# Kernel tuning notes

Measured on AMD Instinct MI355X. Metric: run time of the kernel, lower is better.

The kernel has to match this reference:

```python
import jax, jax.numpy as jnp
import numpy as np

B, T, H, I, O, R = 64, 1024, 1024, 8, 8, 4
NOISE_STD, ALPHA = 0.05, 0.2


def setup_inputs() -> dict:
    key = jax.random.key(0)
    ks = jax.random.split(key, 6)
    return {
        "x": jax.random.normal(ks[0], (B, T, I), jnp.float32),
        "noise": jax.random.normal(ks[1], (B, T, H), jnp.float32),
        "wi": jax.random.normal(ks[2], (I, H), jnp.float32),
        "si": jnp.ones((I,), jnp.float32),
        "m": jax.random.normal(ks[3], (H, R), jnp.float32),
        "n": jax.random.normal(ks[4], (H, R), jnp.float32),
        "b": jnp.zeros((H,), jnp.float32),
        "wo": jax.random.normal(ks[5], (H, O), jnp.float32) / H,
        "so": jnp.ones((O,), jnp.float32),
        "h0": jnp.zeros((H,), jnp.float32),
    }


def reference(x, noise, wi, si, m, n, b, wo, so, h0):
    hidden = h0.shape[0]
    batch = x.shape[0]
    wi_full = wi * si[:, None]          # (I, H): (wi.T * si).T
    wo_full = wo * so                   # (H, O)
    h_init = jnp.broadcast_to(h0, (batch, hidden))
    r_init = jnp.tanh(h_init)           # non_linearity(initial_states)
    # precompute input drive for all steps: (B,T,H) -> scan over time-major
    u = jnp.einsum('bti,ih->tbh', x, wi_full)
    noise_t = jnp.transpose(noise, (1, 0, 2))  # (T,B,H)

    def step(carry, inp):
        h, r = carry
        u_i, nz_i = inp
        rec = (r @ n) @ m.T / hidden                    # low-rank recurrence
        h = h + NOISE_STD * nz_i + ALPHA * (-h + rec + u_i)
        r = jnp.tanh(h + b)
        out = h @ wo_full                               # identity output nonlin
        return (h, r), out

    _, outs = jax.lax.scan(step, (h_init, r_init), (u, noise_t))
    return jnp.transpose(outs, (1, 0, 2))  # (B,T,O)
```

## Files before the change

### kernel.cpp

```cpp
#include <hip/hip_runtime.h>

#define BB 64
#define TT 1024
#define HH 1024
#define II 8
#define OO 8
#define RRK 4
#define NOISE_STD 0.05f
#define ALPHA 0.2f

typedef float v4f __attribute__((ext_vector_type(4)));

#define C2E 2.885390081777927f

template<int CTRL, int RM>
__device__ __forceinline__ float dpp_add(float acc, float src) {
    int s = __builtin_amdgcn_update_dpp(0, __float_as_int(src), CTRL, RM, 0xF, true);
    return acc + __int_as_float(s);
}

__device__ __forceinline__ float wave_sum(float x) {
    x = dpp_add<0xB1, 0xF>(x, x);
    x = dpp_add<0x4E, 0xF>(x, x);
    x = dpp_add<0x141, 0xF>(x, x);
    x = dpp_add<0x140, 0xF>(x, x);
    x = dpp_add<0x142, 0xA>(x, x);
    x = dpp_add<0x143, 0xC>(x, x);
    return x;
}

__device__ __forceinline__ float tanh_from_l2x(float l2x) {
    float e = __builtin_amdgcn_exp2f(l2x);
    float r = __builtin_amdgcn_rcpf(e + 1.0f);
    return fmaf(-2.0f, r, 1.0f);
}

__device__ __forceinline__ void block_sync_lds() {
    asm volatile("s_waitcnt lgkmcnt(0)\n\ts_barrier" ::: "memory");
}

__global__ __launch_bounds__(256)
void prew_kernel(const float* __restrict__ noise, const float* __restrict__ wo,
                 const float* __restrict__ so, float* __restrict__ W) {
    __shared__ __align__(16) float red[2][8][4][8];

    const int tid  = threadIdx.x;
    const int wave = tid >> 6;
    const int lane = tid & 63;
    const int e0   = tid << 2;

    float woa[4][OO];
    {
        float so8[OO];
        #pragma unroll
        for (int o = 0; o < OO; ++o) so8[o] = so[o] * NOISE_STD;
        #pragma unroll
        for (int e = 0; e < 4; ++e) {
            const float4 a4 = *(const float4*)(wo + (e0 + e) * OO);
            const float4 b4 = *(const float4*)(wo + (e0 + e) * OO + 4);
            woa[e][0] = a4.x * so8[0]; woa[e][1] = a4.y * so8[1];
            woa[e][2] = a4.z * so8[2]; woa[e][3] = a4.w * so8[3];
            woa[e][4] = b4.x * so8[4]; woa[e][5] = b4.y * so8[5];
            woa[e][6] = b4.z * so8[6]; woa[e][7] = b4.w * so8[7];
        }
    }

    const int row0 = blockIdx.x * 32;
    #pragma unroll
    for (int ph = 0; ph < 4; ++ph) {
        const int cur   = ph & 1;
        const int rbase = row0 + ph * 8;

        float4 nz[8];
        #pragma unroll
        for (int j = 0; j < 8; ++j)
            nz[j] = *(const float4*)(noise + (size_t)(rbase + j) * HH + e0);

        #pragma unroll
        for (int j = 0; j < 8; ++j) {
            float op[OO];
            #pragma unroll
            for (int o = 0; o < OO; ++o)
                op[o] = fmaf(nz[j].x, woa[0][o], fmaf(nz[j].y, woa[1][o],
                        fmaf(nz[j].z, woa[2][o], nz[j].w * woa[3][o])));
            #pragma unroll
            for (int o = 0; o < OO; ++o) op[o] = wave_sum(op[o]);
            if (lane == 63) {
                *(float4*)&red[cur][j][wave][0] = make_float4(op[0], op[1], op[2], op[3]);
                *(float4*)&red[cur][j][wave][4] = make_float4(op[4], op[5], op[6], op[7]);
            }
        }
        block_sync_lds();
        if (tid < 64) {
            const int j = tid >> 3, o = tid & 7;
            W[(rbase + j) * OO + o] = (red[cur][j][0][o] + red[cur][j][1][o]) +
                                      (red[cur][j][2][o] + red[cur][j][3][o]);
        }
    }
}

__global__ __launch_bounds__(256, 1)
void rnn_seq_kernel(const float* __restrict__ x, const float* __restrict__ noise,
                    const float* __restrict__ wi, const float* __restrict__ si,
                    const float* __restrict__ mM, const float* __restrict__ nM,
                    const float* __restrict__ bv, const float* __restrict__ wo,
                    const float* __restrict__ so, const float* __restrict__ h0,
                    const float* __restrict__ W, float* __restrict__ out) {
    __shared__ __align__(16) float lds_x[(TT + 1) * II];
    __shared__ __align__(16) float lds_W[TT * OO];
    __shared__ __align__(16) float lds_out[TT * OO];
    __shared__ __align__(16) float red[4][4][4];
    __shared__ __align__(16) float redc[4][104];
    __shared__ float ambx[104];

    const int tid  = threadIdx.x;
    const int b    = blockIdx.x;
    const int wave = tid >> 6;
    const int lane = tid & 63;
    const int e0   = tid << 2;
    const int oc   = tid & 7;

    {
        const float4* sx = (const float4*)(x + (size_t)b * (TT * II));
        const float4* sw = (const float4*)(W + (size_t)b * (TT * OO));
        float4* dx = (float4*)lds_x;
        float4* dw = (float4*)lds_W;
        #pragma unroll
        for (int k = 0; k < 8; ++k) {
            dx[k * 256 + tid] = sx[k * 256 + tid];
            dw[k * 256 + tid] = sw[k * 256 + tid];
        }
        if (tid < 2) dx[2048 + tid] = sx[2046 + tid];
    }

    float wia[II][4];
    v4f   wiac[II];
    #pragma unroll
    for (int i = 0; i < II; ++i) {
        const float s  = ALPHA * si[i];
        const float4 w = *(const float4*)(wi + i * HH + e0);
        wia[i][0] = w.x * s; wia[i][1] = w.y * s; wia[i][2] = w.z * s; wia[i][3] = w.w * s;
        wiac[i] = (v4f){wia[i][0], wia[i][1], wia[i][2], wia[i][3]};
    }
    float ma[4][RRK];
    v4f   nrv[4];
    v4f   mac[RRK];
    #pragma unroll
    for (int e = 0; e < 4; ++e) {
        const float4 m4 = *(const float4*)(mM + (e0 + e) * RRK);
        const float4 n4 = *(const float4*)(nM + (e0 + e) * RRK);
        const float cs = ALPHA / (float)HH;
        ma[e][0] = m4.x * cs; ma[e][1] = m4.y * cs; ma[e][2] = m4.z * cs; ma[e][3] = m4.w * cs;
        nrv[e] = (v4f){n4.x, n4.y, n4.z, n4.w};
    }
    #pragma unroll
    for (int q = 0; q < RRK; ++q)
        mac[q] = (v4f){ma[0][q], ma[1][q], ma[2][q], ma[3][q]};

    float woa[4][OO];
    {
        float so8[OO];
        #pragma unroll
        for (int o = 0; o < OO; ++o) so8[o] = so[o];
        #pragma unroll
        for (int e = 0; e < 4; ++e) {
            const float4 a4 = *(const float4*)(wo + (e0 + e) * OO);
            const float4 b4 = *(const float4*)(wo + (e0 + e) * OO + 4);
            woa[e][0] = a4.x * so8[0]; woa[e][1] = a4.y * so8[1];
            woa[e][2] = a4.z * so8[2]; woa[e][3] = a4.w * so8[3];
            woa[e][4] = b4.x * so8[4]; woa[e][5] = b4.y * so8[5];
            woa[e][6] = b4.z * so8[6]; woa[e][7] = b4.w * so8[7];
        }
    }
    v4f tb2e, h, r;
    {
        const v4f b4 = *(const v4f*)(bv + e0);
        tb2e = C2E * b4;
        h = *(const v4f*)(h0 + e0);
        v4f targ = C2E * h;
        r.x = tanh_from_l2x(targ.x); r.y = tanh_from_l2x(targ.y);
        r.z = tanh_from_l2x(targ.z); r.w = tanh_from_l2x(targ.w);
    }

    #pragma unroll
    for (int kg = 0; kg < 26; ++kg) {
        float p[4];
        #pragma unroll
        for (int u = 0; u < 4; ++u) {
            const int k = kg * 4 + u;
            float s;
            if (k < 32) {
                const int q = k >> 3, o = k & 7;
                s = fmaf(ma[0][q], woa[0][o], fmaf(ma[1][q], woa[1][o],
                    fmaf(ma[2][q], woa[2][o], ma[3][q] * woa[3][o])));
            } else if (k < 96) {
                const int i = (k - 32) >> 3, o = k & 7;
                s = fmaf(wia[i][0], woa[0][o], fmaf(wia[i][1], woa[1][o],
                    fmaf(wia[i][2], woa[2][o], wia[i][3] * woa[3][o])));
            } else {
                const int o = k - 96;
                s = fmaf(h.x, woa[0][o], fmaf(h.y, woa[1][o],
                    fmaf(h.z, woa[2][o], h.w * woa[3][o])));
            }
            p[u] = wave_sum(s);
        }
        if (lane == 63)
            *(float4*)&redc[wave][kg * 4] = make_float4(p[0], p[1], p[2], p[3]);
    }
    block_sync_lds();
    if (tid < 104)
        ambx[tid] = (redc[0][tid] + redc[1][tid]) + (redc[2][tid] + redc[3][tid]);
    __syncthreads();

    float Amr[RRK], Bxr[II], y;
    #pragma unroll
    for (int q = 0; q < RRK; ++q) Amr[q] = ambx[q * 8 + oc];
    #pragma unroll
    for (int i = 0; i < II; ++i) Bxr[i] = ambx[32 + i * 8 + oc];
    y = ambx[96 + oc];

    const float* nzp = noise + (size_t)b * (TT * HH) + e0;
    v4f nzb[4];
    #pragma unroll
    for (int j = 0; j < 4; ++j) nzb[j] = *(const v4f*)(nzp + j * HH);

    v4f xqc0 = *(const v4f*)&lds_x[0];
    v4f xqc1 = *(const v4f*)&lds_x[4];
    float wqc = lds_W[oc];

    for (int t0 = 0; t0 < TT; t0 += 4) {
        #pragma unroll
        for (int j = 0; j < 4; ++j) {
            const int t = t0 + j;

            const int tn = t + 1;
            const v4f xqn0 = *(const v4f*)&lds_x[tn * II];
            const v4f xqn1 = *(const v4f*)&lds_x[tn * II + 4];
            const float wqn = lds_W[(tn & (TT - 1)) * OO + oc];

            v4f vpv = r.x * nrv[0];
            vpv += r.y * nrv[1];
            vpv += r.z * nrv[2];
            vpv += r.w * nrv[3];
            float vp0 = wave_sum(vpv.x);
            float vp1 = wave_sum(vpv.y);
            float vp2 = wave_sum(vpv.z);
            float vp3 = wave_sum(vpv.w);
            if (lane == 63)
                *(float4*)&red[j][wave][0] = make_float4(vp0, vp1, vp2, vp3);

            float ybase = fmaf(xqc0.x, Bxr[0], wqc);
            ybase = fmaf(xqc0.y, Bxr[1], ybase);
            ybase = fmaf(xqc0.z, Bxr[2], ybase);
            ybase = fmaf(xqc0.w, Bxr[3], ybase);
            ybase = fmaf(xqc1.x, Bxr[4], ybase);
            ybase = fmaf(xqc1.y, Bxr[5], ybase);
            ybase = fmaf(xqc1.z, Bxr[6], ybase);
            ybase = fmaf(xqc1.w, Bxr[7], ybase);

            v4f auv = xqc0.x * wiac[0];
            auv += xqc0.y * wiac[1];
            auv += xqc0.z * wiac[2];
            auv += xqc0.w * wiac[3];
            auv += xqc1.x * wiac[4];
            auv += xqc1.y * wiac[5];
            auv += xqc1.z * wiac[6];
            auv += xqc1.w * wiac[7];

            block_sync_lds();

            const v4f s0 = *(const v4f*)&red[j][0][0];
            const v4f s1 = *(const v4f*)&red[j][1][0];
            const v4f s2 = *(const v4f*)&red[j][2][0];
            const v4f s3 = *(const v4f*)&red[j][3][0];
            const v4f vs = (s0 + s1) + (s2 + s3);

            v4f acc = auv;
            acc += vs.x * mac[0];
            acc += vs.y * mac[1];
            acc += vs.z * mac[2];
            acc += vs.w * mac[3];
            h = (1.0f - ALPHA) * h + acc;
            h += NOISE_STD * nzb[j];

            {
                float t4 = fmaf(vs.x, Amr[0], ybase);
                t4 = fmaf(vs.y, Amr[1], t4);
                t4 = fmaf(vs.z, Amr[2], t4);
                t4 = fmaf(vs.w, Amr[3], t4);
                y = fmaf(1.0f - ALPHA, y, t4);
                if (tid < OO) lds_out[t * OO + tid] = y;
            }

            nzb[j] = *(const v4f*)(nzp + ((t + 4) & (TT - 1)) * HH);

            {
                v4f targ = C2E * h + tb2e;
                r.x = tanh_from_l2x(targ.x);
                r.y = tanh_from_l2x(targ.y);
                r.z = tanh_from_l2x(targ.z);
                r.w = tanh_from_l2x(targ.w);
            }

            xqc0 = xqn0; xqc1 = xqn1; wqc = wqn;
        }
    }

    __syncthreads();
    {
        float4* dst = (float4*)(out + (size_t)b * (TT * OO));
        const float4* srcv = (const float4*)lds_out;
        #pragma unroll
        for (int k = 0; k < 8; ++k)
            dst[k * 256 + tid] = srcv[k * 256 + tid];
    }
}

extern "C" void kernel_launch(void* const* d_in, const int* in_sizes, int n_in,
                              void* d_out, int out_size, void* d_ws, size_t ws_size,
                              hipStream_t stream) {
    const float* x     = (const float*)d_in[0];
    const float* noise = (const float*)d_in[1];
    const float* wi    = (const float*)d_in[2];
    const float* si    = (const float*)d_in[3];
    const float* mM    = (const float*)d_in[4];
    const float* nM    = (const float*)d_in[5];
    const float* bv    = (const float*)d_in[6];
    const float* wo    = (const float*)d_in[7];
    const float* so    = (const float*)d_in[8];
    const float* h0    = (const float*)d_in[9];
    float* out = (float*)d_out;
    float* W   = (float*)d_ws;

    prew_kernel<<<dim3(2048), dim3(256), 0, stream>>>(noise, wo, so, W);
    rnn_seq_kernel<<<dim3(BB), dim3(256), 0, stream>>>(
        x, noise, wi, si, mM, nM, bv, wo, so, h0, W, out);
}
```

Baseline: 769.7 us.

## Double sequential kernel threads to 512, two hidden units each; prefetch noise in prew

The recurrent kernel now runs 512 threads per batch block, with each thread owning 2 hidden units instead of 4. The cross-wave reduction grows from 4 to 8 partial sums. This halves the per-thread serial work per timestep, mainly the tanh calls and the vector FMAs, and doubles the waves available to hide the per-step noise loads. The cost is an extra LDS read and add per step for the larger reduction, plus more waves taking part in each barrier. Separately, prew_kernel now loads the next phase's noise rows before it reduces the current ones, to overlap that memory traffic with compute.

```diff
diff --git a/kernel.cpp b/kernel.cpp
--- a/kernel.cpp
+++ b/kernel.cpp
@@ -10,6 +10,7 @@
 #define ALPHA 0.2f
 
 typedef float v4f __attribute__((ext_vector_type(4)));
+typedef float v2f __attribute__((ext_vector_type(2)));
 
 #define C2E 2.885390081777927f
 
@@ -66,15 +67,21 @@
     }
 
     const int row0 = blockIdx.x * 32;
+    float4 nz[8], nzn[8];
+    #pragma unroll
+    for (int j = 0; j < 8; ++j)
+        nz[j] = *(const float4*)(noise + (size_t)(row0 + j) * HH + e0);
+
     #pragma unroll
     for (int ph = 0; ph < 4; ++ph) {
         const int cur   = ph & 1;
         const int rbase = row0 + ph * 8;
 
-        float4 nz[8];
-        #pragma unroll
-        for (int j = 0; j < 8; ++j)
-            nz[j] = *(const float4*)(noise + (size_t)(rbase + j) * HH + e0);
+        if (ph < 3) {
+            #pragma unroll
+            for (int j = 0; j < 8; ++j)
+                nzn[j] = *(const float4*)(noise + (size_t)(rbase + 8 + j) * HH + e0);
+        }
 
         #pragma unroll
         for (int j = 0; j < 8; ++j) {
@@ -96,10 +103,12 @@
             W[(rbase + j) * OO + o] = (red[cur][j][0][o] + red[cur][j][1][o]) +
                                       (red[cur][j][2][o] + red[cur][j][3][o]);
         }
-    }
-}
-
-__global__ __launch_bounds__(256, 1)
+        #pragma unroll
+        for (int j = 0; j < 8; ++j) nz[j] = nzn[j];
+    }
+}
+
+__global__ __launch_bounds__(512, 1)
 void rnn_seq_kernel(const float* __restrict__ x, const float* __restrict__ noise,
                     const float* __restrict__ wi, const float* __restrict__ si,
                     const float* __restrict__ mM, const float* __restrict__ nM,
@@ -109,15 +118,15 @@
     __shared__ __align__(16) float lds_x[(TT + 1) * II];
     __shared__ __align__(16) float lds_W[TT * OO];
     __shared__ __align__(16) float lds_out[TT * OO];
-    __shared__ __align__(16) float red[4][4][4];
-    __shared__ __align__(16) float redc[4][104];
+    __shared__ __align__(16) float red[4][8][4];
+    __shared__ __align__(16) float redc[8][104];
     __shared__ float ambx[104];
 
     const int tid  = threadIdx.x;
     const int b    = blockIdx.x;
     const int wave = tid >> 6;
     const int lane = tid & 63;
-    const int e0   = tid << 2;
+    const int e0   = tid << 1;
     const int oc   = tid & 7;
 
     {
@@ -126,60 +135,54 @@
         float4* dx = (float4*)lds_x;
         float4* dw = (float4*)lds_W;
         #pragma unroll
-        for (int k = 0; k < 8; ++k) {
-            dx[k * 256 + tid] = sx[k * 256 + tid];
-            dw[k * 256 + tid] = sw[k * 256 + tid];
+        for (int k = 0; k < 4; ++k) {
+            dx[k * 512 + tid] = sx[k * 512 + tid];
+            dw[k * 512 + tid] = sw[k * 512 + tid];
         }
         if (tid < 2) dx[2048 + tid] = sx[2046 + tid];
     }
 
-    float wia[II][4];
-    v4f   wiac[II];
+    v2f wiac[II];
     #pragma unroll
     for (int i = 0; i < II; ++i) {
         const float s  = ALPHA * si[i];
-        const float4 w = *(const float4*)(wi + i * HH + e0);
-        wia[i][0] = w.x * s; wia[i][1] = w.y * s; wia[i][2] = w.z * s; wia[i][3] = w.w * s;
-        wiac[i] = (v4f){wia[i][0], wia[i][1], wia[i][2], wia[i][3]};
-    }
-    float ma[4][RRK];
-    v4f   nrv[4];
-    v4f   mac[RRK];
-    #pragma unroll
-    for (int e = 0; e < 4; ++e) {
-        const float4 m4 = *(const float4*)(mM + (e0 + e) * RRK);
-        const float4 n4 = *(const float4*)(nM + (e0 + e) * RRK);
+        const v2f w = *(const v2f*)(wi + i * HH + e0);
+        wiac[i] = s * w;
+    }
+    v4f nr0, nr1;
+    v4f ma0, ma1;
+    v2f mac[RRK];
+    {
         const float cs = ALPHA / (float)HH;
-        ma[e][0] = m4.x * cs; ma[e][1] = m4.y * cs; ma[e][2] = m4.z * cs; ma[e][3] = m4.w * cs;
-        nrv[e] = (v4f){n4.x, n4.y, n4.z, n4.w};
-    }
-    #pragma unroll
-    for (int q = 0; q < RRK; ++q)
-        mac[q] = (v4f){ma[0][q], ma[1][q], ma[2][q], ma[3][q]};
-
-    float woa[4][OO];
-    {
-        float so8[OO];
-        #pragma unroll
-        for (int o = 0; o < OO; ++o) so8[o] = so[o];
-        #pragma unroll
-        for (int e = 0; e < 4; ++e) {
+        ma0 = cs * *(const v4f*)(mM + (size_t)e0 * RRK);
+        ma1 = cs * *(const v4f*)(mM + (size_t)(e0 + 1) * RRK);
+        nr0 = *(const v4f*)(nM + (size_t)e0 * RRK);
+        nr1 = *(const v4f*)(nM + (size_t)(e0 + 1) * RRK);
+        mac[0] = (v2f){ma0.x, ma1.x};
+        mac[1] = (v2f){ma0.y, ma1.y};
+        mac[2] = (v2f){ma0.z, ma1.z};
+        mac[3] = (v2f){ma0.w, ma1.w};
+    }
+    float woa[2][OO];
+    {
+        #pragma unroll
+        for (int e = 0; e < 2; ++e) {
             const float4 a4 = *(const float4*)(wo + (e0 + e) * OO);
             const float4 b4 = *(const float4*)(wo + (e0 + e) * OO + 4);
-            woa[e][0] = a4.x * so8[0]; woa[e][1] = a4.y * so8[1];
-            woa[e][2] = a4.z * so8[2]; woa[e][3] = a4.w * so8[3];
-            woa[e][4] = b4.x * so8[4]; woa[e][5] = b4.y * so8[5];
-            woa[e][6] = b4.z * so8[6]; woa[e][7] = b4.w * so8[7];
-        }
-    }
-    v4f tb2e, h, r;
-    {
-        const v4f b4 = *(const v4f*)(bv + e0);
-        tb2e = C2E * b4;
-        h = *(const v4f*)(h0 + e0);
-        v4f targ = C2E * h;
-        r.x = tanh_from_l2x(targ.x); r.y = tanh_from_l2x(targ.y);
-        r.z = tanh_from_l2x(targ.z); r.w = tanh_from_l2x(targ.w);
+            woa[e][0] = a4.x * so[0]; woa[e][1] = a4.y * so[1];
+            woa[e][2] = a4.z * so[2]; woa[e][3] = a4.w * so[3];
+            woa[e][4] = b4.x * so[4]; woa[e][5] = b4.y * so[5];
+            woa[e][6] = b4.z * so[6]; woa[e][7] = b4.w * so[7];
+        }
+    }
+    v2f tb2e, h, r;
+    {
+        const v2f b2 = *(const v2f*)(bv + e0);
+        tb2e = C2E * b2;
+        h = *(const v2f*)(h0 + e0);
+        v2f targ = C2E * h;
+        r.x = tanh_from_l2x(targ.x);
+        r.y = tanh_from_l2x(targ.y);
     }
 
     #pragma unroll
@@ -191,16 +194,15 @@
             float s;
             if (k < 32) {
                 const int q = k >> 3, o = k & 7;
-                s = fmaf(ma[0][q], woa[0][o], fmaf(ma[1][q], woa[1][o],
-                    fmaf(ma[2][q], woa[2][o], ma[3][q] * woa[3][o])));
+                const float m0 = (q == 0) ? ma0.x : (q == 1) ? ma0.y : (q == 2) ? ma0.z : ma0.w;
+                const float m1 = (q == 0) ? ma1.x : (q == 1) ? ma1.y : (q == 2) ? ma1.z : ma1.w;
+                s = fmaf(m0, woa[0][o], m1 * woa[1][o]);
             } else if (k < 96) {
                 const int i = (k - 32) >> 3, o = k & 7;
-                s = fmaf(wia[i][0], woa[0][o], fmaf(wia[i][1], woa[1][o],
-                    fmaf(wia[i][2], woa[2][o], wia[i][3] * woa[3][o])));
+                s = fmaf(wiac[i].x, woa[0][o], wiac[i].y * woa[1][o]);
             } else {
                 const int o = k - 96;
-                s = fmaf(h.x, woa[0][o], fmaf(h.y, woa[1][o],
-                    fmaf(h.z, woa[2][o], h.w * woa[3][o])));
+                s = fmaf(h.x, woa[0][o], h.y * woa[1][o]);
             }
             p[u] = wave_sum(s);
         }
@@ -209,7 +211,8 @@
     }
     block_sync_lds();
     if (tid < 104)
-        ambx[tid] = (redc[0][tid] + redc[1][tid]) + (redc[2][tid] + redc[3][tid]);
+        ambx[tid] = ((redc[0][tid] + redc[1][tid]) + (redc[2][tid] + redc[3][tid])) +
+                    ((redc[4][tid] + redc[5][tid]) + (redc[6][tid] + redc[7][tid]));
     __syncthreads();
 
     float Amr[RRK], Bxr[II], y;
@@ -220,9 +223,9 @@
     y = ambx[96 + oc];
 
     const float* nzp = noise + (size_t)b * (TT * HH) + e0;
-    v4f nzb[4];
-    #pragma unroll
-    for (int j = 0; j < 4; ++j) nzb[j] = *(const v4f*)(nzp + j * HH);
+    v2f nzb[4];
+    #pragma unroll
+    for (int j = 0; j < 4; ++j) nzb[j] = *(const v2f*)(nzp + j * HH);
 
     v4f xqc0 = *(const v4f*)&lds_x[0];
     v4f xqc1 = *(const v4f*)&lds_x[4];
@@ -238,10 +241,8 @@
             const v4f xqn1 = *(const v4f*)&lds_x[tn * II + 4];
             const float wqn = lds_W[(tn & (TT - 1)) * OO + oc];
 
-            v4f vpv = r.x * nrv[0];
-            vpv += r.y * nrv[1];
-            vpv += r.z * nrv[2];
-            vpv += r.w * nrv[3];
+            v4f vpv = r.x * nr0;
+            vpv += r.y * nr1;
             float vp0 = wave_sum(vpv.x);
             float vp1 = wave_sum(vpv.y);
             float vp2 = wave_sum(vpv.z);
@@ -258,7 +259,7 @@
             ybase = fmaf(xqc1.z, Bxr[6], ybase);
             ybase = fmaf(xqc1.w, Bxr[7], ybase);
 
-            v4f auv = xqc0.x * wiac[0];
+            v2f auv = xqc0.x * wiac[0];
             auv += xqc0.y * wiac[1];
             auv += xqc0.z * wiac[2];
             auv += xqc0.w * wiac[3];
@@ -269,13 +270,20 @@
 
             block_sync_lds();
 
-            const v4f s0 = *(const v4f*)&red[j][0][0];
-            const v4f s1 = *(const v4f*)&red[j][1][0];
-            const v4f s2 = *(const v4f*)&red[j][2][0];
-            const v4f s3 = *(const v4f*)&red[j][3][0];
-            const v4f vs = (s0 + s1) + (s2 + s3);
-
-            v4f acc = auv;
+            v4f vs;
+            {
+                const v4f s0 = *(const v4f*)&red[j][0][0];
+                const v4f s1 = *(const v4f*)&red[j][1][0];
+                const v4f s2 = *(const v4f*)&red[j][2][0];
+                const v4f s3 = *(const v4f*)&red[j][3][0];
+                const v4f s4 = *(const v4f*)&red[j][4][0];
+                const v4f s5 = *(const v4f*)&red[j][5][0];
+                const v4f s6 = *(const v4f*)&red[j][6][0];
+                const v4f s7 = *(const v4f*)&red[j][7][0];
+                vs = ((s0 + s1) + (s2 + s3)) + ((s4 + s5) + (s6 + s7));
+            }
+
+            v2f acc = auv;
             acc += vs.x * mac[0];
             acc += vs.y * mac[1];
             acc += vs.z * mac[2];
@@ -292,14 +300,12 @@
                 if (tid < OO) lds_out[t * OO + tid] = y;
             }
 
-            nzb[j] = *(const v4f*)(nzp + ((t + 4) & (TT - 1)) * HH);
+            nzb[j] = *(const v2f*)(nzp + ((t + 4) & (TT - 1)) * HH);
 
             {
-                v4f targ = C2E * h + tb2e;
+                v2f targ = C2E * h + tb2e;
                 r.x = tanh_from_l2x(targ.x);
                 r.y = tanh_from_l2x(targ.y);
-                r.z = tanh_from_l2x(targ.z);
-                r.w = tanh_from_l2x(targ.w);
             }
 
             xqc0 = xqn0; xqc1 = xqn1; wqc = wqn;
@@ -311,8 +317,8 @@
         float4* dst = (float4*)(out + (size_t)b * (TT * OO));
         const float4* srcv = (const float4*)lds_out;
         #pragma unroll
-        for (int k = 0; k < 8; ++k)
-            dst[k * 256 + tid] = srcv[k * 256 + tid];
+        for (int k = 0; k < 4; ++k)
+            dst[k * 512 + tid] = srcv[k * 512 + tid];
     }
 }
 
@@ -333,6 +339,6 @@
     float* W   = (float*)d_ws;
 
     prew_kernel<<<dim3(2048), dim3(256), 0, stream>>>(noise, wo, so, W);
-    rnn_seq_kernel<<<dim3(BB), dim3(256), 0, stream>>>(
+    rnn_seq_kernel<<<dim3(BB), dim3(512), 0, stream>>>(
         x, noise, wi, si, mM, nM, bv, wo, so, h0, W, out);
 }
```

After: 924.8 us. 20.2% more time.

## Precompute fused input+noise drive and run recurrence with one wave per batch

Applied to the files above, without the earlier changes.

A new pre-pass computes the full drive d = alpha*x@wi + noise_std*noise into a 256 MB workspace, along with its projection onto the output weights. The recurrent kernel then uses a single 64-lane wave per batch element, with 16 hidden units per lane. This removes the cross-wave LDS reduction and the barrier from every timestep. Outputs are rebuilt afterwards with a chunked parallel scan over the linear output recurrence. The cost is a large extra global write and read of d, a dependence on workspace size with the old path kept as fallback, and far fewer active waves per CU.

```diff
diff --git a/kernel.cpp b/kernel.cpp
--- a/kernel.cpp
+++ b/kernel.cpp
@@ -29,6 +29,10 @@
     return x;
 }
 
+__device__ __forceinline__ float rl63(float x) {
+    return __int_as_float(__builtin_amdgcn_readlane(__float_as_int(x), 63));
+}
+
 __device__ __forceinline__ float tanh_from_l2x(float l2x) {
     float e = __builtin_amdgcn_exp2f(l2x);
     float r = __builtin_amdgcn_rcpf(e + 1.0f);
@@ -39,9 +43,304 @@
     asm volatile("s_waitcnt lgkmcnt(0)\n\ts_barrier" ::: "memory");
 }
 
+__device__ __forceinline__ void lds_fence() {
+    asm volatile("s_waitcnt lgkmcnt(0)" ::: "memory");
+}
+
+
 __global__ __launch_bounds__(256)
-void prew_kernel(const float* __restrict__ noise, const float* __restrict__ wo,
-                 const float* __restrict__ so, float* __restrict__ W) {
+void pre_d_kernel(const float* __restrict__ x, const float* __restrict__ noise,
+                  const float* __restrict__ wi, const float* __restrict__ si,
+                  const float* __restrict__ wo, const float* __restrict__ so,
+                  float* __restrict__ d, float* __restrict__ sbase) {
+    __shared__ __align__(16) float red[2][8][4][8];
+
+    const int tid  = threadIdx.x;
+    const int wave = tid >> 6;
+    const int lane = tid & 63;
+    const int e0   = tid << 2;
+
+    v4f wia4[II];
+    #pragma unroll
+    for (int i = 0; i < II; ++i)
+        wia4[i] = (ALPHA * si[i]) * *(const v4f*)(wi + (size_t)i * HH + e0);
+
+    float woa[4][OO];
+    #pragma unroll
+    for (int e = 0; e < 4; ++e) {
+        const float4 a4 = *(const float4*)(wo + (e0 + e) * OO);
+        const float4 b4 = *(const float4*)(wo + (e0 + e) * OO + 4);
+        woa[e][0] = a4.x * so[0]; woa[e][1] = a4.y * so[1];
+        woa[e][2] = a4.z * so[2]; woa[e][3] = a4.w * so[3];
+        woa[e][4] = b4.x * so[4]; woa[e][5] = b4.y * so[5];
+        woa[e][6] = b4.z * so[6]; woa[e][7] = b4.w * so[7];
+    }
+
+    const int row0 = blockIdx.x * 32;
+    float4 nz[8], nzn[8];
+    #pragma unroll
+    for (int j = 0; j < 8; ++j)
+        nz[j] = *(const float4*)(noise + (size_t)(row0 + j) * HH + e0);
+
+    #pragma unroll
+    for (int ph = 0; ph < 4; ++ph) {
+        const int cur   = ph & 1;
+        const int rbase = row0 + ph * 8;
+
+        if (ph < 3) {
+            #pragma unroll
+            for (int j = 0; j < 8; ++j)
+                nzn[j] = *(const float4*)(noise + (size_t)(rbase + 8 + j) * HH + e0);
+        }
+
+        #pragma unroll
+        for (int j = 0; j < 8; ++j) {
+            const int row = rbase + j;
+            const float4 xr0 = *(const float4*)(x + (size_t)row * II);
+            const float4 xr1 = *(const float4*)(x + (size_t)row * II + 4);
+            v4f u = xr0.x * wia4[0];
+            u += xr0.y * wia4[1];  u += xr0.z * wia4[2];
+            u += xr0.w * wia4[3];  u += xr1.x * wia4[4];
+            u += xr1.y * wia4[5];  u += xr1.z * wia4[6];
+            u += xr1.w * wia4[7];
+            v4f d4 = u;
+            d4.x = fmaf(NOISE_STD, nz[j].x, d4.x);
+            d4.y = fmaf(NOISE_STD, nz[j].y, d4.y);
+            d4.z = fmaf(NOISE_STD, nz[j].z, d4.z);
+            d4.w = fmaf(NOISE_STD, nz[j].w, d4.w);
+            *(v4f*)(d + (size_t)row * HH + e0) = d4;
+
+            float op[OO];
+            #pragma unroll
+            for (int o = 0; o < OO; ++o)
+                op[o] = fmaf(d4.x, woa[0][o], fmaf(d4.y, woa[1][o],
+                        fmaf(d4.z, woa[2][o], d4.w * woa[3][o])));
+            #pragma unroll
+            for (int o = 0; o < OO; ++o) op[o] = wave_sum(op[o]);
+            if (lane == 63) {
+                *(float4*)&red[cur][j][wave][0] = make_float4(op[0], op[1], op[2], op[3]);
+                *(float4*)&red[cur][j][wave][4] = make_float4(op[4], op[5], op[6], op[7]);
+            }
+        }
+        block_sync_lds();
+        if (tid < 64) {
+            const int j = tid >> 3, o = tid & 7;
+            sbase[(rbase + j) * OO + o] = (red[cur][j][0][o] + red[cur][j][1][o]) +
+                                          (red[cur][j][2][o] + red[cur][j][3][o]);
+        }
+        #pragma unroll
+        for (int j = 0; j < 8; ++j) nz[j] = nzn[j];
+    }
+}
+
+__global__ __launch_bounds__(64, 1)
+void rnn_d_kernel(const float* __restrict__ d, const float* __restrict__ sbase,
+                  const float* __restrict__ mM, const float* __restrict__ nM,
+                  const float* __restrict__ bv, const float* __restrict__ wo,
+                  const float* __restrict__ so, const float* __restrict__ h0,
+                  float* __restrict__ out) {
+    __shared__ __align__(16) float lds_sb[TT * OO];
+    __shared__ __align__(16) float lds_v[TT * RRK];
+    __shared__ __align__(16) float amy[40];
+    __shared__ float chs[8][OO];
+
+    const int lane = threadIdx.x;
+    const int b    = blockIdx.x;
+    const int e0   = lane << 4;
+    const int oc   = lane & 7;
+
+    {
+        const float4* ss = (const float4*)(sbase + (size_t)b * (TT * OO));
+        float4* dsb = (float4*)lds_sb;
+        #pragma unroll
+        for (int k = 0; k < 32; ++k)
+            dsb[k * 64 + lane] = ss[k * 64 + lane];
+    }
+
+    v4f mag[4][RRK];
+    {
+        const float cs = ALPHA / (float)HH;
+        #pragma unroll
+        for (int g = 0; g < 4; ++g) {
+            v4f m0 = cs * *(const v4f*)(mM + (size_t)(e0 + g*4 + 0) * RRK);
+            v4f m1 = cs * *(const v4f*)(mM + (size_t)(e0 + g*4 + 1) * RRK);
+            v4f m2 = cs * *(const v4f*)(mM + (size_t)(e0 + g*4 + 2) * RRK);
+            v4f m3 = cs * *(const v4f*)(mM + (size_t)(e0 + g*4 + 3) * RRK);
+            #pragma unroll
+            for (int q = 0; q < RRK; ++q)
+                mag[g][q] = (v4f){m0[q], m1[q], m2[q], m3[q]};
+        }
+    }
+    v4f h[4], r[4], tb[4];
+    #pragma unroll
+    for (int g = 0; g < 4; ++g) {
+        h[g]  = *(const v4f*)(h0 + e0 + g * 4);
+        tb[g] = C2E * *(const v4f*)(bv + e0 + g * 4);
+        const v4f tg = C2E * h[g];
+        r[g].x = tanh_from_l2x(tg.x); r[g].y = tanh_from_l2x(tg.y);
+        r[g].z = tanh_from_l2x(tg.z); r[g].w = tanh_from_l2x(tg.w);
+    }
+
+    {
+        float acc[40];
+        #pragma unroll
+        for (int k = 0; k < 40; ++k) acc[k] = 0.0f;
+        float so8[OO];
+        #pragma unroll
+        for (int o = 0; o < OO; ++o) so8[o] = so[o];
+        #pragma unroll
+        for (int e = 0; e < 16; ++e) {
+            const int g = e >> 2, eg = e & 3;
+            const float4 a4 = *(const float4*)(wo + (size_t)(e0 + e) * OO);
+            const float4 b4 = *(const float4*)(wo + (size_t)(e0 + e) * OO + 4);
+            float wp[OO];
+            wp[0] = a4.x * so8[0]; wp[1] = a4.y * so8[1];
+            wp[2] = a4.z * so8[2]; wp[3] = a4.w * so8[3];
+            wp[4] = b4.x * so8[4]; wp[5] = b4.y * so8[5];
+            wp[6] = b4.z * so8[6]; wp[7] = b4.w * so8[7];
+            #pragma unroll
+            for (int q = 0; q < RRK; ++q) {
+                const float ms = mag[g][q][eg];
+                #pragma unroll
+                for (int o = 0; o < OO; ++o)
+                    acc[q * 8 + o] = fmaf(ms, wp[o], acc[q * 8 + o]);
+            }
+            const float hs = h[g][eg];
+            #pragma unroll
+            for (int o = 0; o < OO; ++o)
+                acc[32 + o] = fmaf(hs, wp[o], acc[32 + o]);
+        }
+        #pragma unroll
+        for (int k = 0; k < 40; ++k) acc[k] = wave_sum(acc[k]);
+        if (lane == 63) {
+            #pragma unroll
+            for (int k = 0; k < 10; ++k)
+                *(float4*)&amy[k * 4] = make_float4(acc[k*4+0], acc[k*4+1],
+                                                    acc[k*4+2], acc[k*4+3]);
+        }
+    }
+
+    v4f nrv[16];
+    #pragma unroll
+    for (int e = 0; e < 16; ++e)
+        nrv[e] = *(const v4f*)(nM + (size_t)(e0 + e) * RRK);
+
+    const float* dp = d + (size_t)b * (TT * HH) + e0;
+    v4f dA[4], dB[4];
+    #pragma unroll
+    for (int g = 0; g < 4; ++g) {
+        dA[g] = *(const v4f*)(dp + g * 4);
+        dB[g] = *(const v4f*)(dp + (size_t)HH + g * 4);
+    }
+
+#define RNN_STEP(t, D, PF)                                                     \
+    {                                                                          \
+                  \
+        v4f c0 = r[0].x * nrv[0];  c0 += r[0].y * nrv[1];                      \
+        c0 += r[0].z * nrv[2];     c0 += r[0].w * nrv[3];                      \
+        v4f c1 = r[1].x * nrv[4];  c1 += r[1].y * nrv[5];                      \
+        c1 += r[1].z * nrv[6];     c1 += r[1].w * nrv[7];                      \
+        v4f c2 = r[2].x * nrv[8];  c2 += r[2].y * nrv[9];                      \
+        c2 += r[2].z * nrv[10];    c2 += r[2].w * nrv[11];                     \
+        v4f c3 = r[3].x * nrv[12]; c3 += r[3].y * nrv[13];                     \
+        c3 += r[3].z * nrv[14];    c3 += r[3].w * nrv[15];                     \
+        const v4f vp = (c0 + c1) + (c2 + c3);                                  \
+             \
+        const float s0 = wave_sum(vp.x);                                       \
+        const float s1 = wave_sum(vp.y);                                       \
+        const float s2 = wave_sum(vp.z);                                       \
+        const float s3 = wave_sum(vp.w);                                       \
+        if (lane == 63)                                                        \
+            *(float4*)&lds_v[(t) * RRK] = make_float4(s0, s1, s2, s3);         \
+        const float v0 = rl63(s0);                                             \
+        const float v1 = rl63(s1);                                             \
+        const float v2 = rl63(s2);                                             \
+        const float v3 = rl63(s3);                                             \
+          \
+        _Pragma("unroll")                                                      \
+        for (int g = 0; g < 4; ++g) {                                          \
+            v4f a = D[g];                                                      \
+            a += v0 * mag[g][0];   a += v1 * mag[g][1];                        \
+            a += v2 * mag[g][2];   a += v3 * mag[g][3];                        \
+            h[g] = (1.0f - ALPHA) * h[g] + a;                                  \
+        }                                                                      \
+                     \
+        if (PF) {                                                              \
+            const float* np = dp + (size_t)((t) + 2) * HH;                     \
+            _Pragma("unroll")                                                  \
+            for (int g = 0; g < 4; ++g) D[g] = *(const v4f*)(np + g * 4);      \
+        }                                                                      \
+                                                          \
+        _Pragma("unroll")                                                      \
+        for (int g = 0; g < 4; ++g) {                                          \
+            const v4f tg = C2E * h[g] + tb[g];                                 \
+            r[g].x = tanh_from_l2x(tg.x); r[g].y = tanh_from_l2x(tg.y);        \
+            r[g].z = tanh_from_l2x(tg.z); r[g].w = tanh_from_l2x(tg.w);        \
+        }                                                                      \
+    }
+
+    for (int t = 0; t < TT - 2; t += 2) {
+        RNN_STEP(t,     dA, 1)
+        RNN_STEP(t + 1, dB, 1)
+    }
+    RNN_STEP(TT - 2, dA, 0)
+    RNN_STEP(TT - 1, dB, 0)
+#undef RNN_STEP
+
+    lds_fence();
+
+    float Amr[RRK];
+    #pragma unroll
+    for (int q = 0; q < RRK; ++q) Amr[q] = amy[q * 8 + oc];
+
+    const int c  = lane >> 3;
+    const int tc = c * 128;
+    float a128;
+    {
+        float a = 1.0f - ALPHA;
+        #pragma unroll
+        for (int k = 0; k < 7; ++k) a = a * a;
+        a128 = a;
+    }
+
+    auto step_s = [&](int t) -> float {
+        const v4f vv = *(const v4f*)&lds_v[t * RRK];
+        float s = lds_sb[t * OO + oc];
+        s = fmaf(vv.x, Amr[0], s); s = fmaf(vv.y, Amr[1], s);
+        s = fmaf(vv.z, Amr[2], s); s = fmaf(vv.w, Amr[3], s);
+        return s;
+    };
+
+    float L = 0.0f;
+    #pragma unroll 4
+    for (int jt = 0; jt < 128; ++jt)
+        L = fmaf(1.0f - ALPHA, L, step_s(tc + jt));
+    chs[c][oc] = L;
+    lds_fence();
+    if (lane < OO) {
+        float Y = amy[32 + lane];
+        #pragma unroll
+        for (int c2 = 0; c2 < 8; ++c2) {
+            const float Lc = chs[c2][lane];
+            chs[c2][lane] = Y;
+            Y = fmaf(a128, Y, Lc);
+        }
+    }
+    lds_fence();
+    float yv = chs[c][oc];
+    float* ob = out + (size_t)b * (TT * OO);
+    #pragma unroll 4
+    for (int jt = 0; jt < 128; ++jt) {
+        const int t = tc + jt;
+        yv = fmaf(1.0f - ALPHA, yv, step_s(t));
+        ob[t * OO + oc] = yv;
+    }
+}
+
+
+__global__ __launch_bounds__(256)
+void prew_fb(const float* __restrict__ noise, const float* __restrict__ wo,
+             const float* __restrict__ so, float* __restrict__ W) {
     __shared__ __align__(16) float red[2][8][4][8];
 
     const int tid  = threadIdx.x;
@@ -66,16 +365,20 @@
     }
 
     const int row0 = blockIdx.x * 32;
+    float4 nz[8], nzn[8];
+    #pragma unroll
+    for (int j = 0; j < 8; ++j)
+        nz[j] = *(const float4*)(noise + (size_t)(row0 + j) * HH + e0);
+
     #pragma unroll
     for (int ph = 0; ph < 4; ++ph) {
         const int cur   = ph & 1;
         const int rbase = row0 + ph * 8;
-
-        float4 nz[8];
-        #pragma unroll
-        for (int j = 0; j < 8; ++j)
-            nz[j] = *(const float4*)(noise + (size_t)(rbase + j) * HH + e0);
-
+        if (ph < 3) {
+            #pragma unroll
+            for (int j = 0; j < 8; ++j)
+                nzn[j] = *(const float4*)(noise + (size_t)(rbase + 8 + j) * HH + e0);
+        }
         #pragma unroll
         for (int j = 0; j < 8; ++j) {
             float op[OO];
@@ -96,16 +399,18 @@
             W[(rbase + j) * OO + o] = (red[cur][j][0][o] + red[cur][j][1][o]) +
                                       (red[cur][j][2][o] + red[cur][j][3][o]);
         }
+        #pragma unroll
+        for (int j = 0; j < 8; ++j) nz[j] = nzn[j];
     }
 }
 
 __global__ __launch_bounds__(256, 1)
-void rnn_seq_kernel(const float* __restrict__ x, const float* __restrict__ noise,
-                    const float* __restrict__ wi, const float* __restrict__ si,
-                    const float* __restrict__ mM, const float* __restrict__ nM,
-                    const float* __restrict__ bv, const float* __restrict__ wo,
-                    const float* __restrict__ so, const float* __restrict__ h0,
-                    const float* __restrict__ W, float* __restrict__ out) {
+void rnn_fb(const float* __restrict__ x, const float* __restrict__ noise,
+            const float* __restrict__ wi, const float* __restrict__ si,
+            const float* __restrict__ mM, const float* __restrict__ nM,
+            const float* __restrict__ bv, const float* __restrict__ wo,
+            const float* __restrict__ so, const float* __restrict__ h0,
+            const float* __restrict__ W, float* __restrict__ out) {
     __shared__ __align__(16) float lds_x[(TT + 1) * II];
     __shared__ __align__(16) float lds_W[TT * OO];
     __shared__ __align__(16) float lds_out[TT * OO];
@@ -159,27 +464,24 @@
 
     float woa[4][OO];
     {
-        float so8[OO];
-        #pragma unroll
-        for (int o = 0; o < OO; ++o) so8[o] = so[o];
         #pragma unroll
         for (int e = 0; e < 4; ++e) {
             const float4 a4 = *(const float4*)(wo + (e0 + e) * OO);
             const float4 b4 = *(const float4*)(wo + (e0 + e) * OO + 4);
-            woa[e][0] = a4.x * so8[0]; woa[e][1] = a4.y * so8[1];
-            woa[e][2] = a4.z * so8[2]; woa[e][3] = a4.w * so8[3];
-            woa[e][4] = b4.x * so8[4]; woa[e][5] = b4.y * so8[5];
-            woa[e][6] = b4.z * so8[6]; woa[e][7] = b4.w * so8[7];
-        }
-    }
-    v4f tb2e, h, r;
+            woa[e][0] = a4.x * so[0]; woa[e][1] = a4.y * so[1];
+            woa[e][2] = a4.z * so[2]; woa[e][3] = a4.w * so[3];
+            woa[e][4] = b4.x * so[4]; woa[e][5] = b4.y * so[5];
+            woa[e][6] = b4.z * so[6]; woa[e][7] = b4.w * so[7];
+        }
+    }
+    v4f tb2e, h, rr;
     {
         const v4f b4 = *(const v4f*)(bv + e0);
         tb2e = C2E * b4;
         h = *(const v4f*)(h0 + e0);
         v4f targ = C2E * h;
-        r.x = tanh_from_l2x(targ.x); r.y = tanh_from_l2x(targ.y);
-        r.z = tanh_from_l2x(targ.z); r.w = tanh_from_l2x(targ.w);
+        rr.x = tanh_from_l2x(targ.x); rr.y = tanh_from_l2x(targ.y);
+        rr.z = tanh_from_l2x(targ.z); rr.w = tanh_from_l2x(targ.w);
     }
 
     #pragma unroll
@@ -232,16 +534,15 @@
         #pragma unroll
         for (int j = 0; j < 4; ++j) {
             const int t = t0 + j;
-
             const int tn = t + 1;
             const v4f xqn0 = *(const v4f*)&lds_x[tn * II];
             const v4f xqn1 = *(const v4f*)&lds_x[tn * II + 4];
             const float wqn = lds_W[(tn & (TT - 1)) * OO + oc];
 
-            v4f vpv = r.x * nrv[0];
-            vpv += r.y * nrv[1];
-            vpv += r.z * nrv[2];
-            vpv += r.w * nrv[3];
+            v4f vpv = rr.x * nrv[0];
+            vpv += rr.y * nrv[1];
+            vpv += rr.z * nrv[2];
+            vpv += rr.w * nrv[3];
             float vp0 = wave_sum(vpv.x);
             float vp1 = wave_sum(vpv.y);
             float vp2 = wave_sum(vpv.z);
@@ -296,12 +597,11 @@
 
             {
                 v4f targ = C2E * h + tb2e;
-                r.x = tanh_from_l2x(targ.x);
-                r.y = tanh_from_l2x(targ.y);
-                r.z = tanh_from_l2x(targ.z);
-                r.w = tanh_from_l2x(targ.w);
+                rr.x = tanh_from_l2x(targ.x);
+                rr.y = tanh_from_l2x(targ.y);
+                rr.z = tanh_from_l2x(targ.z);
+                rr.w = tanh_from_l2x(targ.w);
             }
-
             xqc0 = xqn0; xqc1 = xqn1; wqc = wqn;
         }
     }
@@ -330,9 +630,21 @@
     const float* so    = (const float*)d_in[8];
     const float* h0    = (const float*)d_in[9];
     float* out = (float*)d_out;
-    float* W   = (float*)d_ws;
-
-    prew_kernel<<<dim3(2048), dim3(256), 0, stream>>>(noise, wo, so, W);
-    rnn_seq_kernel<<<dim3(BB), dim3(256), 0, stream>>>(
-        x, noise, wi, si, mM, nM, bv, wo, so, h0, W, out);
-}
+
+    const size_t needD = (size_t)BB * TT * HH * sizeof(float);
+    const size_t needS = (size_t)BB * TT * OO * sizeof(float);
+
+    if (ws_size >= needD + needS) {
+        float* dbuf = (float*)d_ws;
+        float* sb   = dbuf + (size_t)BB * TT * HH;
+        pre_d_kernel<<<dim3(2048), dim3(256), 0, stream>>>(
+            x, noise, wi, si, wo, so, dbuf, sb);
+        rnn_d_kernel<<<dim3(BB), dim3(64), 0, stream>>>(
+            dbuf, sb, mM, nM, bv, wo, so, h0, out);
+    } else {
+        float* W = (float*)d_ws;
+        prew_fb<<<dim3(2048), dim3(256), 0, stream>>>(noise, wo, so, W);
+        rnn_fb<<<dim3(BB), dim3(256), 0, stream>>>(
+            x, noise, wi, si, mM, nM, bv, wo, so, h0, W, out);
+    }
+}
```

After: 932.7 us. 21.2% more time.
